# Kernel optimization log

Hardware: AMD Instinct MI355X
Metric: run time of the kernel (lower is better)

Reference implementation:

```python
import jax, jax.numpy as jnp
import numpy as np

KS = 3          # kernel_size
DILS = (1, 2)   # dilation list
NH = 8          # num_heads


def _unfold(x, k, r):
    # x: [B, d, H, W] -> [B, d, k*k, H, W], matching nn.Unfold(k, dilation=r,
    # padding=r*(k-1)//2): kernel positions enumerated row-major over (kh, kw).
    B, d, H, W = x.shape
    pad = r * (k - 1) // 2
    xp = jnp.pad(x, ((0, 0), (0, 0), (pad, pad), (pad, pad)))
    patches = [xp[:, :, i * r:i * r + H, j * r:j * r + W]
               for i in range(k) for j in range(k)]
    return jnp.stack(patches, axis=2)


def setup_inputs() -> dict:
    key = jax.random.key(0)
    k1, k2, k3, k4 = jax.random.split(key, 4)
    B, H, W, C = 2, 160, 160, 128
    return {
        "x": jax.random.normal(k1, (B, H, W, C), dtype=jnp.float32),
        "qkv_w": jax.random.normal(k2, (3 * C, C), dtype=jnp.float32) * 0.05,
        "proj_w": jax.random.normal(k3, (C, C), dtype=jnp.float32) * 0.05,
        "proj_b": jax.random.normal(k4, (C,), dtype=jnp.float32) * 0.05,
    }


def reference(x, qkv_w, proj_w, proj_b):
    B, H, W, C = x.shape
    nd = len(DILS)
    hd = C // NH               # head_dim = 16
    d = C // nd                # channels per dilation group = 64
    h = d // hd                # heads per dilation group = 4
    scale = hd ** -0.5
    L = H * W

    xc = x.transpose(0, 3, 1, 2)                       # [B, C, H, W]
    qkv = jnp.einsum('bchw,oc->bohw', xc, qkv_w)       # 1x1 conv, no bias
    qkv = qkv.reshape(B, 3, nd, d, H, W)

    outs = []
    for i, r in enumerate(DILS):
        q, kk, v = qkv[:, 0, i], qkv[:, 1, i], qkv[:, 2, i]   # [B, d, H, W]
        qh = q.reshape(B, h, hd, L).transpose(0, 1, 3, 2)      # [B, h, L, hd]
        ku = _unfold(kk, KS, r).reshape(B, h, hd, KS * KS, L)  # [B, h, hd, 9, L]
        vu = _unfold(v, KS, r).reshape(B, h, hd, KS * KS, L)
        attn = jnp.einsum('bhld,bhdkl->bhlk', qh, ku) * scale  # [B, h, L, 9]
        attn = jax.nn.softmax(attn, axis=-1)
        o = jnp.einsum('bhlk,bhdkl->bhld', attn, vu)           # [B, h, L, hd]
        outs.append(o.transpose(0, 2, 1, 3).reshape(B, H, W, d))

    y = jnp.concatenate(outs, axis=-1)                  # [B, H, W, C]
    return y @ proj_w.T + proj_b
```

## Files before the change

kernel.cpp:

```cpp
#include <hip/hip_runtime.h>
#include <cstdint>

#define HW_ 160
#define NPIX (2*160*160)

typedef __attribute__((ext_vector_type(8))) short short8;
typedef __attribute__((ext_vector_type(4))) float f32x4;

__device__ __forceinline__ unsigned short f2bf(float f) {
  union { float f; unsigned u; } v; v.f = f;
  unsigned r = v.u + 0x7fffu + ((v.u >> 16) & 1u);
  return (unsigned short)(r >> 16);
}
__device__ __forceinline__ float bflo(unsigned u) {
  union { unsigned u; float f; } v; v.u = u << 16; return v.f;
}
__device__ __forceinline__ float bfhi(unsigned u) {
  union { unsigned u; float f; } v; v.u = u & 0xffff0000u; return v.f;
}

__device__ __forceinline__ short8 cvt8(const float4& x0, const float4& x1) {
  short8 h;
  h[0] = (short)f2bf(x0.x); h[1] = (short)f2bf(x0.y);
  h[2] = (short)f2bf(x0.z); h[3] = (short)f2bf(x0.w);
  h[4] = (short)f2bf(x1.x); h[5] = (short)f2bf(x1.y);
  h[6] = (short)f2bf(x1.z); h[7] = (short)f2bf(x1.w);
  return h;
}

__global__ __launch_bounds__(256)
void cvt_w(const float* __restrict__ qw, unsigned short* __restrict__ dst) {
  int i = (blockIdx.x * 256 + threadIdx.x) * 4;
  float4 v = *(const float4*)(qw + i);
  dst[i] = f2bf(v.x); dst[i + 1] = f2bf(v.y);
  dst[i + 2] = f2bf(v.z); dst[i + 3] = f2bf(v.w);
}

__global__ __launch_bounds__(256, 4)
void qkv_gemm(const float* __restrict__ x, const unsigned short* __restrict__ wq,
              unsigned int* __restrict__ qt2) {
  __shared__ short As[64 * 128];
  const int t = threadIdx.x;
  const int p0 = blockIdx.x * 64;
  const int og = blockIdx.y;

  const float* A = x + (size_t)p0 * 128;
#pragma unroll
  for (int i = 0; i < 4; ++i) {
    int f = t + i * 256;
    int row = f >> 4;
    float4 x0 = *(const float4*)(A + f * 8);
    float4 x1 = *(const float4*)(A + f * 8 + 4);
    int dst = (row * 256 + (f & 15) * 16) ^ ((row & 7) << 4);
    *(short8*)((char*)As + dst) = cvt8(x0, x1);
  }
  __syncthreads();

  const int lane = t & 63, wv = t >> 6;
  const int wp = wv & 1, wc = wv >> 1;
  const int lr = lane & 15, lk = lane >> 4;

  short8 af[2][4];
#pragma unroll
  for (int m = 0; m < 2; ++m)
#pragma unroll
    for (int kk = 0; kk < 4; ++kk) {
      int row = wp * 32 + m * 16 + lr;
      int off = (row * 256 + kk * 64 + lk * 16) ^ ((row & 7) << 4);
      af[m][kk] = *(const short8*)((const char*)As + off);
    }

#pragma unroll
  for (int it = 0; it < 3; ++it) {
    const int o0 = og * 192 + it * 64 + wc * 32;
    short8 bfr[2][4];
#pragma unroll
    for (int n = 0; n < 2; ++n) {
      const unsigned short* wr_ = wq + (size_t)(o0 + n * 16 + lr) * 128;
#pragma unroll
      for (int kk = 0; kk < 4; ++kk)
        bfr[n][kk] = *(const short8*)(wr_ + kk * 32 + lk * 8);
    }
    f32x4 acc[2][2];
#pragma unroll
    for (int n = 0; n < 2; ++n)
#pragma unroll
      for (int m = 0; m < 2; ++m) acc[n][m] = 0.f;
#pragma unroll
    for (int kk = 0; kk < 4; ++kk)
#pragma unroll
      for (int n = 0; n < 2; ++n)
#pragma unroll
        for (int m = 0; m < 2; ++m)
          acc[n][m] = __builtin_amdgcn_mfma_f32_16x16x32_bf16(
              bfr[n][kk], af[m][kk], acc[n][m], 0, 0, 0);
#pragma unroll
    for (int n = 0; n < 2; ++n)
#pragma unroll
      for (int m = 0; m < 2; ++m) {
        int ob = o0 + n * 16 + lk * 4;
        int p = p0 + wp * 32 + m * 16 + lr;
        unsigned u0 = ((unsigned)f2bf(acc[n][m][1]) << 16) | f2bf(acc[n][m][0]);
        unsigned u1 = ((unsigned)f2bf(acc[n][m][3]) << 16) | f2bf(acc[n][m][2]);
        qt2[(size_t)(ob >> 1) * NPIX + p] = u0;
        qt2[(size_t)((ob >> 1) + 1) * NPIX + p] = u1;
      }
  }
}

__global__ __launch_bounds__(512, 4)
void attn_proj(const unsigned int* __restrict__ qt2,
               const float* __restrict__ wp_f32,
               const float* __restrict__ bias, float* __restrict__ C) {
  __shared__ short Ys[64 * 128];
  __shared__ short Ws[128 * 128];
  const int t = threadIdx.x;
  const int p0 = blockIdx.x * 64;

#pragma unroll
  for (int i = 0; i < 4; ++i) {
    int f = t + i * 512;
    int row = f >> 4;
    float4 x0 = *(const float4*)(wp_f32 + f * 8);
    float4 x1 = *(const float4*)(wp_f32 + f * 8 + 4);
    int dst = (row * 256 + (f & 15) * 16) ^ ((row & 7) << 4);
    *(short8*)((char*)Ws + dst) = cvt8(x0, x1);
  }

  const int lane = t & 63, wv = t >> 6;
  const int dil = wv >> 2, head = wv & 3;
  const int r = dil ? 2 : 1;
  const int p = p0 + lane;
  const int rem = p % (HW_ * HW_);
  const int yy = rem / HW_;
  const int xx = rem - yy * HW_;
  const int brow2 = (dil * 64 + head * 16) >> 1;

  const unsigned int* qp = qt2 + (size_t)brow2 * NPIX + p;
  float q[16];
#pragma unroll
  for (int c2 = 0; c2 < 8; ++c2) {
    unsigned u = qp[(size_t)c2 * NPIX];
    q[2 * c2] = bflo(u); q[2 * c2 + 1] = bfhi(u);
  }

  int np[9];
  bool val[9];
#pragma unroll
  for (int jy = 0; jy < 3; ++jy)
#pragma unroll
    for (int jx = 0; jx < 3; ++jx) {
      const int j = jy * 3 + jx;
      const int dy = (jy - 1) * r, dx = (jx - 1) * r;
      val[j] = ((unsigned)(yy + dy) < HW_) && ((unsigned)(xx + dx) < HW_);
      int q_ = p + dy * HW_ + dx;
      np[j] = min(max(q_, 0), NPIX - 1);
    }

  float l[9];
#pragma unroll
  for (int j = 0; j < 9; ++j) l[j] = 0.f;
  const unsigned int* kp = qt2 + (size_t)(64 + brow2) * NPIX;
#pragma unroll
  for (int c2 = 0; c2 < 8; ++c2) {
    const unsigned int* rp = kp + (size_t)c2 * NPIX;
    const float qa = q[2 * c2], qb = q[2 * c2 + 1];
#pragma unroll
    for (int j = 0; j < 9; ++j) {
      unsigned u = rp[np[j]];
      l[j] += qa * bflo(u) + qb * bfhi(u);
    }
  }
#pragma unroll
  for (int j = 0; j < 9; ++j) l[j] = val[j] ? l[j] * 0.25f : 0.f;

  float mx = l[0];
#pragma unroll
  for (int j = 1; j < 9; ++j) mx = fmaxf(mx, l[j]);
  float e[9], s = 0.f;
#pragma unroll
  for (int j = 0; j < 9; ++j) { e[j] = __expf(l[j] - mx); s += e[j]; }
#pragma unroll
  for (int j = 0; j < 9; ++j) if (!val[j]) e[j] = 0.f;
  const float inv = 1.0f / s;

  float o[16];
#pragma unroll
  for (int c = 0; c < 16; ++c) o[c] = 0.f;
  const unsigned int* vp = qt2 + (size_t)(128 + brow2) * NPIX;
#pragma unroll
  for (int c2 = 0; c2 < 8; ++c2) {
    const unsigned int* rp = vp + (size_t)c2 * NPIX;
#pragma unroll
    for (int j = 0; j < 9; ++j) {
      unsigned u = rp[np[j]];
      o[2 * c2] += e[j] * bflo(u);
      o[2 * c2 + 1] += e[j] * bfhi(u);
    }
  }

  {
    short8 h0, h1;
#pragma unroll
    for (int c = 0; c < 8; ++c) h0[c] = (short)f2bf(o[c] * inv);
#pragma unroll
    for (int c = 0; c < 8; ++c) h1[c] = (short)f2bf(o[c + 8] * inv);
    int colb = (dil * 64 + head * 16) * 2;
    int base = (lane * 256 + colb) ^ ((lane & 7) << 4);
    *(short8*)((char*)Ys + base) = h0;
    int base2 = (lane * 256 + colb + 16) ^ ((lane & 7) << 4);
    *(short8*)((char*)Ys + base2) = h1;
  }
  __syncthreads();

  const int wq_ = wv & 3, wo = wv >> 2;
  const int lr = lane & 15, lk = lane >> 4;

  short8 a[4];
#pragma unroll
  for (int kk = 0; kk < 4; ++kk) {
    int row = wq_ * 16 + lr;
    int off = (row * 256 + kk * 64 + lk * 16) ^ ((row & 7) << 4);
    a[kk] = *(const short8*)((const char*)Ys + off);
  }

  f32x4 acc[4];
#pragma unroll
  for (int n = 0; n < 4; ++n) acc[n] = 0.f;
#pragma unroll
  for (int kk = 0; kk < 4; ++kk) {
    short8 b[4];
#pragma unroll
    for (int n = 0; n < 4; ++n) {
      int row = wo * 64 + n * 16 + lr;
      int off = (row * 256 + kk * 64 + lk * 16) ^ ((row & 7) << 4);
      b[n] = *(const short8*)((const char*)Ws + off);
    }
#pragma unroll
    for (int n = 0; n < 4; ++n)
      acc[n] = __builtin_amdgcn_mfma_f32_16x16x32_bf16(a[kk], b[n], acc[n], 0, 0, 0);
  }

#pragma unroll
  for (int n = 0; n < 4; ++n) {
    int ccol = wo * 64 + n * 16 + lr;
    float bv = bias[ccol];
    int crow = p0 + wq_ * 16 + lk * 4;
#pragma unroll
    for (int i = 0; i < 4; ++i)
      C[(size_t)(crow + i) * 128 + ccol] = acc[n][i] + bv;
  }
}

extern "C" void kernel_launch(void* const* d_in, const int* in_sizes, int n_in,
                              void* d_out, int out_size, void* d_ws, size_t ws_size,
                              hipStream_t stream) {
  const float* x      = (const float*)d_in[0];
  const float* qkv_w  = (const float*)d_in[1];
  const float* proj_w = (const float*)d_in[2];
  const float* proj_b = (const float*)d_in[3];
  float* out = (float*)d_out;

  unsigned int* qt2 = (unsigned int*)d_ws;
  unsigned short* wqbf = (unsigned short*)(qt2 + (size_t)192 * NPIX);

  cvt_w<<<48, 256, 0, stream>>>(qkv_w, wqbf);

  qkv_gemm<<<dim3(NPIX / 64, 2), 256, 0, stream>>>(x, wqbf, qt2);

  attn_proj<<<NPIX / 64, 512, 0, stream>>>(qt2, proj_w, proj_b, out);
}
```

Before: 137.6 us.

## Pack QKV as 4-channel uint2 planes and split GEMM over more blocks

The intermediate QKV buffer changes from 2-channel uint32 planes to 4-channel uint2 planes. The attention gathers now issue half as many 8-byte loads per neighbor instead of 4-byte ones. The QKV GEMM drops the shared-memory staging of x and loads and converts activations straight into registers. It also launches 6 output-channel blocks instead of looping 3 times inside 2 blocks, which raises parallelism but makes each x tile be read and converted 6 times instead of 2.

```diff
diff --git a/kernel.cpp b/kernel.cpp
--- a/kernel.cpp
+++ b/kernel.cpp
@@ -38,78 +38,64 @@
 
 __global__ __launch_bounds__(256, 4)
 void qkv_gemm(const float* __restrict__ x, const unsigned short* __restrict__ wq,
-              unsigned int* __restrict__ qt2) {
-  __shared__ short As[64 * 128];
+              uint2* __restrict__ qt4) {
   const int t = threadIdx.x;
-  const int p0 = blockIdx.x * 64;
-  const int og = blockIdx.y;
-
-  const float* A = x + (size_t)p0 * 128;
-#pragma unroll
-  for (int i = 0; i < 4; ++i) {
-    int f = t + i * 256;
-    int row = f >> 4;
-    float4 x0 = *(const float4*)(A + f * 8);
-    float4 x1 = *(const float4*)(A + f * 8 + 4);
-    int dst = (row * 256 + (f & 15) * 16) ^ ((row & 7) << 4);
-    *(short8*)((char*)As + dst) = cvt8(x0, x1);
-  }
-  __syncthreads();
-
   const int lane = t & 63, wv = t >> 6;
   const int wp = wv & 1, wc = wv >> 1;
   const int lr = lane & 15, lk = lane >> 4;
+  const int p0 = blockIdx.x * 64;
+  const int o0 = blockIdx.y * 64 + wc * 32;
+
+  short8 bfr[2][4];
+#pragma unroll
+  for (int n = 0; n < 2; ++n) {
+    const unsigned short* wr_ = wq + (size_t)(o0 + n * 16 + lr) * 128 + lk * 8;
+#pragma unroll
+    for (int kk = 0; kk < 4; ++kk)
+      bfr[n][kk] = *(const short8*)(wr_ + kk * 32);
+  }
 
   short8 af[2][4];
 #pragma unroll
-  for (int m = 0; m < 2; ++m)
+  for (int m = 0; m < 2; ++m) {
+    const float* xp = x + (size_t)(p0 + wp * 32 + m * 16 + lr) * 128 + lk * 8;
 #pragma unroll
     for (int kk = 0; kk < 4; ++kk) {
-      int row = wp * 32 + m * 16 + lr;
-      int off = (row * 256 + kk * 64 + lk * 16) ^ ((row & 7) << 4);
-      af[m][kk] = *(const short8*)((const char*)As + off);
-    }
-
-#pragma unroll
-  for (int it = 0; it < 3; ++it) {
-    const int o0 = og * 192 + it * 64 + wc * 32;
-    short8 bfr[2][4];
-#pragma unroll
-    for (int n = 0; n < 2; ++n) {
-      const unsigned short* wr_ = wq + (size_t)(o0 + n * 16 + lr) * 128;
-#pragma unroll
-      for (int kk = 0; kk < 4; ++kk)
-        bfr[n][kk] = *(const short8*)(wr_ + kk * 32 + lk * 8);
-    }
-    f32x4 acc[2][2];
+      float4 a0 = *(const float4*)(xp + kk * 32);
+      float4 a1 = *(const float4*)(xp + kk * 32 + 4);
+      af[m][kk] = cvt8(a0, a1);
+    }
+  }
+
+  f32x4 acc[2][2];
+#pragma unroll
+  for (int n = 0; n < 2; ++n)
+#pragma unroll
+    for (int m = 0; m < 2; ++m) acc[n][m] = 0.f;
+#pragma unroll
+  for (int kk = 0; kk < 4; ++kk)
 #pragma unroll
     for (int n = 0; n < 2; ++n)
 #pragma unroll
-      for (int m = 0; m < 2; ++m) acc[n][m] = 0.f;
-#pragma unroll
-    for (int kk = 0; kk < 4; ++kk)
-#pragma unroll
-      for (int n = 0; n < 2; ++n)
-#pragma unroll
-        for (int m = 0; m < 2; ++m)
-          acc[n][m] = __builtin_amdgcn_mfma_f32_16x16x32_bf16(
-              bfr[n][kk], af[m][kk], acc[n][m], 0, 0, 0);
-#pragma unroll
-    for (int n = 0; n < 2; ++n)
-#pragma unroll
-      for (int m = 0; m < 2; ++m) {
-        int ob = o0 + n * 16 + lk * 4;
-        int p = p0 + wp * 32 + m * 16 + lr;
-        unsigned u0 = ((unsigned)f2bf(acc[n][m][1]) << 16) | f2bf(acc[n][m][0]);
-        unsigned u1 = ((unsigned)f2bf(acc[n][m][3]) << 16) | f2bf(acc[n][m][2]);
-        qt2[(size_t)(ob >> 1) * NPIX + p] = u0;
-        qt2[(size_t)((ob >> 1) + 1) * NPIX + p] = u1;
-      }
-  }
+      for (int m = 0; m < 2; ++m)
+        acc[n][m] = __builtin_amdgcn_mfma_f32_16x16x32_bf16(
+            bfr[n][kk], af[m][kk], acc[n][m], 0, 0, 0);
+
+#pragma unroll
+  for (int n = 0; n < 2; ++n)
+#pragma unroll
+    for (int m = 0; m < 2; ++m) {
+      int ob = o0 + n * 16 + lk * 4;
+      int p = p0 + wp * 32 + m * 16 + lr;
+      uint2 u;
+      u.x = ((unsigned)f2bf(acc[n][m][1]) << 16) | f2bf(acc[n][m][0]);
+      u.y = ((unsigned)f2bf(acc[n][m][3]) << 16) | f2bf(acc[n][m][2]);
+      qt4[(size_t)(ob >> 2) * NPIX + p] = u;
+    }
 }
 
 __global__ __launch_bounds__(512, 4)
-void attn_proj(const unsigned int* __restrict__ qt2,
+void attn_proj(const uint2* __restrict__ qt4,
                const float* __restrict__ wp_f32,
                const float* __restrict__ bias, float* __restrict__ C) {
   __shared__ short Ys[64 * 128];
@@ -134,14 +120,15 @@
   const int rem = p % (HW_ * HW_);
   const int yy = rem / HW_;
   const int xx = rem - yy * HW_;
-  const int brow2 = (dil * 64 + head * 16) >> 1;
-
-  const unsigned int* qp = qt2 + (size_t)brow2 * NPIX + p;
+  const int brow4 = dil * 16 + head * 4;
+
+  const uint2* qp = qt4 + (size_t)brow4 * NPIX + p;
   float q[16];
 #pragma unroll
-  for (int c2 = 0; c2 < 8; ++c2) {
-    unsigned u = qp[(size_t)c2 * NPIX];
-    q[2 * c2] = bflo(u); q[2 * c2 + 1] = bfhi(u);
+  for (int c4 = 0; c4 < 4; ++c4) {
+    uint2 u = qp[(size_t)c4 * NPIX];
+    q[4 * c4]     = bflo(u.x); q[4 * c4 + 1] = bfhi(u.x);
+    q[4 * c4 + 2] = bflo(u.y); q[4 * c4 + 3] = bfhi(u.y);
   }
 
   int np[9];
@@ -160,15 +147,16 @@
   float l[9];
 #pragma unroll
   for (int j = 0; j < 9; ++j) l[j] = 0.f;
-  const unsigned int* kp = qt2 + (size_t)(64 + brow2) * NPIX;
-#pragma unroll
-  for (int c2 = 0; c2 < 8; ++c2) {
-    const unsigned int* rp = kp + (size_t)c2 * NPIX;
-    const float qa = q[2 * c2], qb = q[2 * c2 + 1];
+  const uint2* kp = qt4 + (size_t)(32 + brow4) * NPIX;
+#pragma unroll
+  for (int c4 = 0; c4 < 4; ++c4) {
+    const uint2* rp = kp + (size_t)c4 * NPIX;
+    const float qa = q[4 * c4], qb = q[4 * c4 + 1];
+    const float qc = q[4 * c4 + 2], qd = q[4 * c4 + 3];
 #pragma unroll
     for (int j = 0; j < 9; ++j) {
-      unsigned u = rp[np[j]];
-      l[j] += qa * bflo(u) + qb * bfhi(u);
+      uint2 u = rp[np[j]];
+      l[j] += qa * bflo(u.x) + qb * bfhi(u.x) + qc * bflo(u.y) + qd * bfhi(u.y);
     }
   }
 #pragma unroll
@@ -187,15 +175,17 @@
   float o[16];
 #pragma unroll
   for (int c = 0; c < 16; ++c) o[c] = 0.f;
-  const unsigned int* vp = qt2 + (size_t)(128 + brow2) * NPIX;
-#pragma unroll
-  for (int c2 = 0; c2 < 8; ++c2) {
-    const unsigned int* rp = vp + (size_t)c2 * NPIX;
+  const uint2* vp = qt4 + (size_t)(64 + brow4) * NPIX;
+#pragma unroll
+  for (int c4 = 0; c4 < 4; ++c4) {
+    const uint2* rp = vp + (size_t)c4 * NPIX;
 #pragma unroll
     for (int j = 0; j < 9; ++j) {
-      unsigned u = rp[np[j]];
-      o[2 * c2] += e[j] * bflo(u);
-      o[2 * c2 + 1] += e[j] * bfhi(u);
+      uint2 u = rp[np[j]];
+      o[4 * c4]     += e[j] * bflo(u.x);
+      o[4 * c4 + 1] += e[j] * bfhi(u.x);
+      o[4 * c4 + 2] += e[j] * bflo(u.y);
+      o[4 * c4 + 3] += e[j] * bfhi(u.y);
     }
   }
 
@@ -261,12 +251,12 @@
   const float* proj_b = (const float*)d_in[3];
   float* out = (float*)d_out;
 
-  unsigned int* qt2 = (unsigned int*)d_ws;
-  unsigned short* wqbf = (unsigned short*)(qt2 + (size_t)192 * NPIX);
+  uint2* qt4 = (uint2*)d_ws;
+  unsigned short* wqbf = (unsigned short*)(qt4 + (size_t)96 * NPIX);
 
   cvt_w<<<48, 256, 0, stream>>>(qkv_w, wqbf);
 
-  qkv_gemm<<<dim3(NPIX / 64, 2), 256, 0, stream>>>(x, wqbf, qt2);
-
-  attn_proj<<<NPIX / 64, 512, 0, stream>>>(qt2, proj_w, proj_b, out);
-}
+  qkv_gemm<<<dim3(NPIX / 64, 6), 256, 0, stream>>>(x, wqbf, qt4);
+
+  attn_proj<<<NPIX / 64, 512, 0, stream>>>(qt4, proj_w, proj_b, out);
+}
```

Result: slower. 157.3 us (+14.3%).
